# Kernel tuning notes

Hardware: AMD Instinct MI355X
Metric: run time of the kernel (lower is better)

## Reference

```python
import jax, jax.numpy as jnp
import numpy as np

B, S, D, H = 2, 2048, 1024, 16
DK = D // H

def setup_inputs() -> dict:
    key = jax.random.key(0)
    k1, k2, k3 = jax.random.split(key, 3)
    std = 2.0 / (D + 3 * D)
    x = jax.random.normal(k1, (B, S, D), dtype=jnp.float32)
    W_qkv = jax.random.normal(k2, (3 * D, D), dtype=jnp.float32) * std
    W_out = jax.random.normal(k3, (D, D), dtype=jnp.float32) * (2.0 / (2 * D))
    return {"x": x, "W_qkv": W_qkv, "W_out": W_out}

def reference(x, W_qkv, W_out):
    # fused QKV projection: [..., d_in] x [d_out, d_in] -> [..., d_out]
    proj = jnp.einsum('bsd,ed->bse', x, W_qkv)               # [B,S,3*H*DK]
    proj = proj.reshape(B, S, 3, H, DK)
    q = proj[:, :, 0].transpose(0, 2, 1, 3)                  # [B,H,S,DK]
    k = proj[:, :, 1].transpose(0, 2, 1, 3)
    v = proj[:, :, 2].transpose(0, 2, 1, 3)
    scores = jnp.einsum('bhnd,bhmd->bhnm', q, k) / jnp.sqrt(jnp.float32(DK))
    causal = jnp.tril(jnp.ones((S, S), dtype=bool))
    scores = jnp.where(causal, scores, -jnp.inf)
    attn = jax.nn.softmax(scores, axis=-1)
    out = jnp.einsum('bhnm,bhmd->bhnd', attn, v)             # [B,H,S,DK]
    out = out.transpose(0, 2, 1, 3).reshape(B, S, H * DK)
    return jnp.einsum('bsd,ed->bse', out, W_out)             # [B,S,D]
```

## Files before the change

### kernel.cpp

```cpp
#include <hip/hip_runtime.h>
#include <hip/hip_bf16.h>
#include <stdint.h>

typedef __attribute__((ext_vector_type(8)))  __bf16 bf16x8;
typedef __attribute__((ext_vector_type(8)))  short  short8;
typedef __attribute__((ext_vector_type(4)))  float  f32x4;
typedef __attribute__((ext_vector_type(16))) float  f32x16;

#define MFMA16(a, b, c) __builtin_amdgcn_mfma_f32_16x16x32_bf16((a), (b), (c), 0, 0, 0)
#define MFMA32(a, b, c) __builtin_amdgcn_mfma_f32_32x32x16_bf16((a), (b), (c), 0, 0, 0)

__device__ __forceinline__ unsigned short f32_bf16(float f) {
  union { float f; unsigned u; } v; v.f = f;
  unsigned r = v.u + 0x7FFFu + ((v.u >> 16) & 1u);
  return (unsigned short)(r >> 16);
}

__device__ __forceinline__ float fast_exp2(float x) {
#if __has_builtin(__builtin_amdgcn_exp2f)
  return __builtin_amdgcn_exp2f(x);
#else
  return __expf(x * 0.69314718f);
#endif
}

__device__ __forceinline__ void gload16(const unsigned short* g, unsigned short* l) {
  __builtin_amdgcn_global_load_lds(
      (const __attribute__((address_space(1))) unsigned int*)(g),
      (__attribute__((address_space(3))) unsigned int*)(l), 16, 0, 0);
}

__global__ void cvt3_kernel(const float* __restrict__ a, int na4,
                            const float* __restrict__ b, int nb4,
                            const float* __restrict__ c, int nc4,
                            unsigned short* __restrict__ oa,
                            unsigned short* __restrict__ ob,
                            unsigned short* __restrict__ oc) {
  int total = na4 + nb4 + nc4;
  for (int i = blockIdx.x * blockDim.x + threadIdx.x; i < total; i += gridDim.x * blockDim.x) {
    const float* src; unsigned short* dst; int j = i;
    if (j < na4) { src = a; dst = oa; }
    else if (j - na4 < nb4) { j -= na4; src = b; dst = ob; }
    else { j -= na4 + nb4; src = c; dst = oc; }
    float4 v = reinterpret_cast<const float4*>(src)[j];
    ushort4 o4;
    o4.x = f32_bf16(v.x); o4.y = f32_bf16(v.y);
    o4.z = f32_bf16(v.z); o4.w = f32_bf16(v.w);
    reinterpret_cast<ushort4*>(dst)[j] = o4;
  }
}

__global__ __launch_bounds__(512, 2) void gemm_qkv_8ph(const unsigned short* __restrict__ A,
                                                       const unsigned short* __restrict__ Bm,
                                                       unsigned short* __restrict__ qkv) {
  extern __shared__ unsigned short SM[];
  const int tid  = threadIdx.x;
  const int lane = tid & 63;
  const int w    = tid >> 6;
  const int wr   = w >> 2, wc = w & 3;
  const int l16  = lane & 15, lh = lane >> 4;
  const int sw   = l16 & 7;
  const int m0   = blockIdx.y * 256;
  const int n0   = blockIdx.x * 256;

  f32x4 acc[8][4];
#pragma unroll
  for (int mi = 0; mi < 8; ++mi)
#pragma unroll
    for (int ni = 0; ni < 4; ++ni) acc[mi][ni] = 0.f;

  const int r0 = tid >> 3,         h0 = (tid & 7) ^ (r0 & 7);
  const int r1 = (tid + 512) >> 3, h1 = (tid & 7) ^ (r1 & 7);
  const unsigned short* Asrc[2][2];
  const unsigned short* Bsrc[2][2];
  Asrc[0][0] = A + (size_t)(m0 + r0) * 1024 + h0 * 8;
  Asrc[0][1] = A + (size_t)(m0 + r1) * 1024 + h1 * 8;
  Asrc[1][0] = A + (size_t)(m0 + 128 + r0) * 1024 + h0 * 8;
  Asrc[1][1] = A + (size_t)(m0 + 128 + r1) * 1024 + h1 * 8;
  Bsrc[0][0] = Bm + (size_t)(n0 + r0) * 1024 + h0 * 8;
  Bsrc[0][1] = Bm + (size_t)(n0 + r1) * 1024 + h1 * 8;
  Bsrc[1][0] = Bm + (size_t)(n0 + 128 + r0) * 1024 + h0 * 8;
  Bsrc[1][1] = Bm + (size_t)(n0 + 128 + r1) * 1024 + h1 * 8;
  const int ld0 = (w * 64) * 8;
  const int ld1 = (512 + w * 64) * 8;

#define STAGE_A(buf, h, U) do { \
    gload16(Asrc[h][0] + (U) * 64, SM + (buf) * 32768 + (h) * 8192 + ld0); \
    gload16(Asrc[h][1] + (U) * 64, SM + (buf) * 32768 + (h) * 8192 + ld1); } while (0)
#define STAGE_B(buf, h, U) do { \
    gload16(Bsrc[h][0] + (U) * 64, SM + (buf) * 32768 + 16384 + (h) * 8192 + ld0); \
    gload16(Bsrc[h][1] + (U) * 64, SM + (buf) * 32768 + 16384 + (h) * 8192 + ld1); } while (0)

  STAGE_A(0, 0, 0); STAGE_A(0, 1, 0);
  STAGE_B(0, 0, 0); STAGE_B(0, 1, 0);
  STAGE_B(1, 0, 1); STAGE_B(1, 1, 1);
  asm volatile("s_waitcnt vmcnt(4)" ::: "memory");
  __builtin_amdgcn_s_barrier();

  const int NT = 16;
#pragma unroll 2
  for (int U = 0; U < NT; ++U) {
    const int b = U & 1;
    const unsigned short* Ab = SM + b * 32768 + wr * 8192;
    const unsigned short* Bb = SM + b * 32768 + 16384 + (wc >> 1) * 8192;
    const int rB = (wc & 1) * 64;
    bf16x8 bfr[4][2], af[2][2];

#define LDA(i, j) (*(const bf16x8*)(Ab + (((i) * 16 + l16) * 8 + (((j) * 4 + lh) ^ sw)) * 8))
#define LDB(n, j) (*(const bf16x8*)(Bb + (((rB + (n) * 16 + l16)) * 8 + (((j) * 4 + lh) ^ sw)) * 8))
#define PHASE_MFMA(p) \
    __builtin_amdgcn_s_setprio(1); \
    _Pragma("unroll") \
    for (int n = 0; n < 4; ++n) { \
      acc[2*(p)][n]   = MFMA16(af[0][0], bfr[n][0], acc[2*(p)][n]); \
      acc[2*(p)][n]   = MFMA16(af[0][1], bfr[n][1], acc[2*(p)][n]); \
      acc[2*(p)+1][n] = MFMA16(af[1][0], bfr[n][0], acc[2*(p)+1][n]); \
      acc[2*(p)+1][n] = MFMA16(af[1][1], bfr[n][1], acc[2*(p)+1][n]); \
    } \
    __builtin_amdgcn_s_setprio(0);

    af[0][0] = LDA(0, 0); af[0][1] = LDA(0, 1);
    af[1][0] = LDA(1, 0); af[1][1] = LDA(1, 1);
#pragma unroll
    for (int n = 0; n < 4; ++n) { bfr[n][0] = LDB(n, 0); bfr[n][1] = LDB(n, 1); }
    if (U + 1 < NT) STAGE_A(b ^ 1, 0, U + 1);
    __builtin_amdgcn_s_barrier();
    PHASE_MFMA(0)
    __builtin_amdgcn_s_barrier();
    af[0][0] = LDA(2, 0); af[0][1] = LDA(2, 1);
    af[1][0] = LDA(3, 0); af[1][1] = LDA(3, 1);
    if (U + 1 < NT) STAGE_A(b ^ 1, 1, U + 1);
    __builtin_amdgcn_s_barrier();
    PHASE_MFMA(1)
    __builtin_amdgcn_s_barrier();
    af[0][0] = LDA(4, 0); af[0][1] = LDA(4, 1);
    af[1][0] = LDA(5, 0); af[1][1] = LDA(5, 1);
    if (U + 2 < NT) STAGE_B(b, 0, U + 2);
    __builtin_amdgcn_s_barrier();
    PHASE_MFMA(2)
    __builtin_amdgcn_s_barrier();
    af[0][0] = LDA(6, 0); af[0][1] = LDA(6, 1);
    af[1][0] = LDA(7, 0); af[1][1] = LDA(7, 1);
    if (U + 2 < NT) STAGE_B(b, 1, U + 2);
    __builtin_amdgcn_s_barrier();
    PHASE_MFMA(3)
    asm volatile("s_waitcnt vmcnt(4)" ::: "memory");
    __builtin_amdgcn_s_barrier();
#undef LDA
#undef LDB
#undef PHASE_MFMA
  }

  __syncthreads();
  unsigned short* Ep = SM + w * 8192;
  const int gn0 = n0 + wc * 64;
  const int cc  = gn0 >> 10;
  const int hh2 = (gn0 & 1023) >> 6;
  const int gm0 = m0 + wr * 128;
  const int bb2 = gm0 >> 11;
  const int ss0 = gm0 & 2047;
  const int bh2 = bb2 * 16 + hh2;

  if (cc < 2) {
    const float qsc = (cc == 0) ? 0.18033688f : 1.0f;
#pragma unroll
    for (int mi = 0; mi < 8; ++mi)
#pragma unroll
      for (int ni = 0; ni < 4; ++ni)
#pragma unroll
        for (int r = 0; r < 4; ++r) {
          int row = mi * 16 + lh * 4 + r;
          int col = (ni * 16 + l16) ^ (lh << 3);
          Ep[row * 64 + col] = f32_bf16(acc[mi][ni][r] * qsc);
        }
    unsigned short* qk = qkv + (((size_t)cc * 32 + bh2) * 2048 + ss0) * 64;
#pragma unroll
    for (int it = 0; it < 16; ++it) {
      int ci = it * 64 + lane;
      int row = ci >> 3, c = ci & 7;
      short8 vv = *(const short8*)(Ep + row * 64 + ((c ^ ((row >> 2) & 3)) * 8));
      *(short8*)(qk + (size_t)row * 64 + c * 8) = vv;
    }
  } else {
#pragma unroll
    for (int mi = 0; mi < 8; ++mi)
#pragma unroll
      for (int ni = 0; ni < 4; ++ni) {
        int dk = ni * 16 + l16;
        int ssl = mi * 16 + lh * 4;
        unsigned lo, hi;
        asm("v_cvt_pk_bf16_f32 %0, %1, %2" : "=v"(lo) : "v"(acc[mi][ni][0]), "v"(acc[mi][ni][1]));
        asm("v_cvt_pk_bf16_f32 %0, %1, %2" : "=v"(hi) : "v"(acc[mi][ni][2]), "v"(acc[mi][ni][3]));
        int off = dk * 128 + (ssl ^ ((dk & 7) << 3));
        *(uint2*)(Ep + off) = make_uint2(lo, hi);
      }
    unsigned short* vt = qkv + (size_t)8388608 + (size_t)bh2 * 64 * 2048 + ss0;
#pragma unroll
    for (int it = 0; it < 16; ++it) {
      int ci = it * 64 + lane;
      int dk = ci >> 4, c = ci & 15;
      short8 vv = *(const short8*)(Ep + dk * 128 + ((c ^ (dk & 7)) * 8));
      *(short8*)(vt + (size_t)dk * 2048 + c * 8) = vv;
    }
  }
#undef STAGE_A
#undef STAGE_B
}

__global__ __launch_bounds__(256) void gemm_out(const unsigned short* __restrict__ A,
                                                const unsigned short* __restrict__ Bm,
                                                float* __restrict__ C,
                                                int M, int N, int K) {
  extern __shared__ unsigned short SM[];
  unsigned short* As = SM;
  unsigned short* Bs = SM + 2048;
  const int tid  = threadIdx.x;
  const int lane = tid & 63;
  const int wid  = tid >> 6;
  const int l16  = lane & 15, lh = lane >> 4;
  const int m0   = blockIdx.y * 64;
  const int n0   = blockIdx.x * 128;

  f32x4 acc[4][2];
#pragma unroll
  for (int mi = 0; mi < 4; ++mi)
#pragma unroll
    for (int ni = 0; ni < 2; ++ni) acc[mi][ni] = 0.f;

  const unsigned short* aSrc = A + (size_t)(m0 + (tid >> 2)) * K + (tid & 3) * 8;
  const unsigned short* b0   = Bm + (size_t)(n0 + (tid >> 2)) * K + (tid & 3) * 8;
  const unsigned short* b1   = Bm + (size_t)(n0 + 64 + (tid >> 2)) * K + (tid & 3) * 8;
  const int dA  = wid * 512;
  const int dB0 = wid * 512;
  const int dB1 = 2048 + wid * 512;

  for (int k0 = 0; k0 < K; k0 += 32) {
    __syncthreads();
    gload16(aSrc + k0, As + dA);
    gload16(b0 + k0, Bs + dB0);
    gload16(b1 + k0, Bs + dB1);
    __syncthreads();
    bf16x8 af[4], bfr[2];
#pragma unroll
    for (int mi = 0; mi < 4; ++mi)
      af[mi] = *(const bf16x8*)(As + (mi * 16 + l16) * 32 + lh * 8);
#pragma unroll
    for (int ni = 0; ni < 2; ++ni)
      bfr[ni] = *(const bf16x8*)(Bs + (wid * 32 + ni * 16 + l16) * 32 + lh * 8);
#pragma unroll
    for (int mi = 0; mi < 4; ++mi)
#pragma unroll
      for (int ni = 0; ni < 2; ++ni)
        acc[mi][ni] = MFMA16(af[mi], bfr[ni], acc[mi][ni]);
  }

  __syncthreads();
  float* Ef = (float*)SM + wid * 2048;
#pragma unroll
  for (int mi = 0; mi < 4; ++mi)
#pragma unroll
    for (int ni = 0; ni < 2; ++ni)
#pragma unroll
      for (int r = 0; r < 4; ++r) {
        int row = mi * 16 + lh * 4 + r;
        int col = (ni * 16 + l16) ^ ((row & 7) << 2);
        Ef[row * 32 + col] = acc[mi][ni][r];
      }
#pragma unroll
  for (int it = 0; it < 8; ++it) {
    int ci = it * 64 + lane;
    int row = ci >> 3, c4 = ci & 7;
    float4 vv = *(const float4*)(Ef + row * 32 + ((c4 * 4) ^ ((row & 7) << 2)));
    *(float4*)(&C[(size_t)(m0 + row) * N + n0 + wid * 32 + c4 * 4]) = vv;
  }
}

__device__ const signed char JQT[48] = {31,31,30,15, 30,29,29,28,14, 28,27,27,26,13, 26,25,25,24,12,
                                        24,23,23,22,11, 22,21,21,20,10, 20,19,19,18, 9, 18,17,17,16, 8,
                                        16, 7, 6, 5, 4, 3, 2, 1, 0};
__device__ const signed char JS0[48] = { 0,16, 0, 0, 16, 0,15, 0, 0, 15, 0,14, 0, 0, 14, 0,13, 0, 0,
                                        13, 0,12, 0, 0, 12, 0,11, 0, 0, 11, 0,10, 0, 0, 10, 0, 9, 0, 0,
                                         9, 0, 0, 0, 0, 0, 0, 0, 0};
__device__ const signed char JNT[48] = {16,16,16,16, 15,15,15,15,15, 14,14,14,14,14, 13,13,13,13,13,
                                        12,12,12,12,12, 11,11,11,11,11, 10,10,10,10,10,  9, 9, 9, 9, 9,
                                         8, 8, 7, 6, 5, 4, 3, 2, 1};
__device__ const signed char JSL[48] = {30,31,28,-1, 29,26,27,24,-1, 25,22,23,20,-1, 21,18,19,16,-1,
                                        17,14,15,12,-1, 13,10,11, 8,-1,  9, 6, 7, 4,-1,  5, 2, 3, 0,-1,
                                         1,-1,-1,-1,-1,-1,-1,-1,-1};

__global__ __launch_bounds__(256) void attn_kernel(const unsigned short* __restrict__ Qg,
                                                   const unsigned short* __restrict__ Kg,
                                                   const unsigned short* __restrict__ Vtg,
                                                   unsigned short* __restrict__ Og,
                                                   char* __restrict__ parts) {
  __shared__ unsigned short Ks[2][64 * 64];
  __shared__ unsigned short Vs[2][64 * 64];

  const int tid  = threadIdx.x;
  const int lane = tid & 63;
  const int w    = tid >> 6;
  const int wq   = w & 1, wkv = w >> 1;
  const int l31  = lane & 31, hi = lane >> 5;
  const int rx0  = (l31 ^ (l31 >> 3)) & 7;

  const int jb   = blockIdx.x >> 5;
  const int bh   = blockIdx.x & 31;
  const int qt   = JQT[jb];
  const int ts0  = JS0[jb];
  const int tend = ts0 + JNT[jb];
  const int slot = JSL[jb];
  const int bb   = bh >> 4, hh = bh & 15;
  const int qb   = qt * 64;
  const int qcol = qb + wq * 32 + l31;

  const unsigned short* Qh = Qg + (size_t)bh * (2048 * 64);
  const unsigned short* Kh = Kg + (size_t)bh * (2048 * 64);
  const unsigned short* Vh = Vtg + (size_t)bh * (64 * 2048);

  bf16x8 qf[4];
#pragma unroll
  for (int ks = 0; ks < 4; ++ks)
    qf[ks] = *(const bf16x8*)(Qh + (size_t)qcol * 64 + ks * 16 + hi * 8);

  f32x16 o0 = 0.f, o1 = 0.f;
  float mreg = 0.f, ll = 0.f;

  const int sA = tid, sB = tid + 256;
  const int rA = sA >> 3, hA = (sA & 7) ^ ((rA ^ (rA >> 3)) & 7);
  const int rB = sB >> 3, hB = (sB & 7) ^ ((rB ^ (rB >> 3)) & 7);
  const unsigned short* kSrcA = Kh + rA * 64 + hA * 8;
  const unsigned short* kSrcB = Kh + rB * 64 + hB * 8;
  const unsigned short* vSrcA = Vh + (size_t)rA * 2048 + hA * 8;
  const unsigned short* vSrcB = Vh + (size_t)rB * 2048 + hB * 8;
  const int ldsA = (w * 64) * 8;
  const int ldsB = (256 + w * 64) * 8;

  gload16(kSrcA + (size_t)(ts0 * 64) * 64, &Ks[0][ldsA]);
  gload16(kSrcB + (size_t)(ts0 * 64) * 64, &Ks[0][ldsB]);
  gload16(vSrcA + ts0 * 64, &Vs[0][ldsA]);
  gload16(vSrcB + ts0 * 64, &Vs[0][ldsB]);
  __syncthreads();

  const unsigned short* kA = kSrcA + (size_t)(ts0 + 1) * 4096;
  const unsigned short* kB = kSrcB + (size_t)(ts0 + 1) * 4096;
  const unsigned short* vA = vSrcA + (ts0 + 1) * 64;
  const unsigned short* vB = vSrcB + (ts0 + 1) * 64;

  for (int t = ts0; t < tend; ++t) {
    const int kv0 = t * 64;
    const int cur = (t - ts0) & 1;
    if (t + 1 < tend) {
      gload16(kA, &Ks[cur ^ 1][ldsA]);
      gload16(kB, &Ks[cur ^ 1][ldsB]);
      gload16(vA, &Vs[cur ^ 1][ldsA]);
      gload16(vB, &Vs[cur ^ 1][ldsB]);
      kA += 4096; kB += 4096; vA += 64; vB += 64;
    }
    const unsigned short* Kb = Ks[cur];
    const unsigned short* Vb = Vs[cur];

    f32x16 s = 0.f;
    const int kvl = wkv * 32 + l31;
#pragma unroll
    for (int ks = 0; ks < 4; ++ks) {
      int c = (ks * 2 + hi) ^ rx0 ^ (wkv << 2);
      bf16x8 ka = *(const bf16x8*)(Kb + kvl * 64 + c * 8);
      s = MFMA32(ka, qf[ks], s);
    }

    if (t == qt) {
#pragma unroll
      for (int r = 0; r < 16; ++r) {
        int kvp = kv0 + wkv * 32 + (r & 3) + 8 * (r >> 2) + 4 * hi;
        if (kvp > qcol) s[r] = -__builtin_inff();
      }
    }

    float pm = fmaxf(fmaxf(s[0], s[1]), s[2]);
    pm = fmaxf(fmaxf(pm, s[3]), s[4]);
    pm = fmaxf(fmaxf(pm, s[5]), s[6]);
    pm = fmaxf(fmaxf(pm, s[7]), s[8]);
    pm = fmaxf(fmaxf(pm, s[9]), s[10]);
    pm = fmaxf(fmaxf(pm, s[11]), s[12]);
    pm = fmaxf(fmaxf(pm, s[13]), s[14]);
    pm = fmaxf(pm, s[15]);
    if (!__all(pm <= mreg + 8.f)) {
      float t0 = fmaxf(pm, __shfl_xor(pm, 32));
      float mn = fmaxf(mreg, t0);
      float esc = fast_exp2(mreg - mn);
      mreg = mn; ll *= esc;
#pragma unroll
      for (int r = 0; r < 16; ++r) { o0[r] *= esc; o1[r] *= esc; }
    }

    float p[16];
#pragma unroll
    for (int r = 0; r < 16; ++r) p[r] = fast_exp2(s[r] - mreg);
    float ps = ((p[0] + p[1]) + (p[2] + p[3])) + ((p[4] + p[5]) + (p[6] + p[7]))
             + ((p[8] + p[9]) + (p[10] + p[11])) + ((p[12] + p[13]) + (p[14] + p[15]));
    ps += __shfl_xor(ps, 32);
    ll += ps;

    bf16x8 pf[2];
#pragma unroll
    for (int ks = 0; ks < 2; ++ks) {
      const int off = ks * 8;
      unsigned a1, b1, a2, b2;
      asm("v_cvt_pk_bf16_f32 %0, %1, %2" : "=v"(a1) : "v"(p[off + 0]), "v"(p[off + 1]));
      asm("v_cvt_pk_bf16_f32 %0, %1, %2" : "=v"(b1) : "v"(p[off + 4]), "v"(p[off + 5]));
      asm("v_cvt_pk_bf16_f32 %0, %1, %2" : "=v"(a2) : "v"(p[off + 2]), "v"(p[off + 3]));
      asm("v_cvt_pk_bf16_f32 %0, %1, %2" : "=v"(b2) : "v"(p[off + 6]), "v"(p[off + 7]));
      asm("v_permlane32_swap_b32 %0, %1" : "+v"(a1), "+v"(b1));
      asm("v_permlane32_swap_b32 %0, %1" : "+v"(a2), "+v"(b2));
      union { unsigned u[4]; bf16x8 f; } fr;
      fr.u[0] = a1; fr.u[1] = a2; fr.u[2] = b1; fr.u[3] = b2;
      pf[ks] = fr.f;
    }

#pragma unroll
    for (int ks = 0; ks < 2; ++ks) {
      int cbase = wkv * 4 + ks * 2 + hi;
      bf16x8 va0 = *(const bf16x8*)(Vb + l31 * 64 + (cbase ^ rx0) * 8);
      bf16x8 va1 = *(const bf16x8*)(Vb + (32 + l31) * 64 + (cbase ^ rx0 ^ 4) * 8);
      o0 = MFMA32(va0, pf[ks], o0);
      o1 = MFMA32(va1, pf[ks], o1);
    }
    __syncthreads();
  }

  float* oxch = (float*)Ks;
  float* lmx  = (float*)Vs;
  if (wkv == 1) {
    float* dst = oxch + wq * 2048;
#pragma unroll
    for (int r = 0; r < 16; ++r) {
      int d0 = (r & 3) + 8 * (r >> 2) + 4 * hi;
      dst[d0 * 32 + l31] = o0[r];
      dst[(32 + d0) * 32 + l31] = o1[r];
    }
    if (hi == 0) { lmx[wq * 64 + l31] = ll; lmx[wq * 64 + 32 + l31] = mreg; }
  }
  __syncthreads();
  if (wkv == 0) {
    float lB = lmx[wq * 64 + l31];
    float mB = lmx[wq * 64 + 32 + l31];
    float mx = fmaxf(mreg, mB);
    float wA = fast_exp2(mreg - mx), wB = fast_exp2(mB - mx);
    float lT = ll * wA + lB * wB;
    float inv = (slot < 0) ? (1.f / lT) : 1.f;
    float sA2 = wA * inv, sB2 = wB * inv;
    const float* src = oxch + wq * 2048;
    unsigned short* slab = (unsigned short*)((char*)Vs + 1024) + wq * 2048;
#pragma unroll
    for (int i = 0; i < 8; ++i) {
      int r = 2 * i;
      int d0 = (r & 3) + 8 * (r >> 2) + 4 * hi;
      float x0 = o0[r] * sA2 + src[d0 * 32 + l31] * sB2;
      float x1 = o0[r + 1] * sA2 + src[(d0 + 1) * 32 + l31] * sB2;
      float y0 = o1[r] * sA2 + src[(32 + d0) * 32 + l31] * sB2;
      float y1 = o1[r + 1] * sA2 + src[(33 + d0) * 32 + l31] * sB2;
      unsigned u0, u1;
      asm("v_cvt_pk_bf16_f32 %0, %1, %2" : "=v"(u0) : "v"(x0), "v"(x1));
      asm("v_cvt_pk_bf16_f32 %0, %1, %2" : "=v"(u1) : "v"(y0), "v"(y1));
      *(unsigned*)(slab + l31 * 64 + (((d0 >> 3) ^ (l31 & 7)) * 8) + (d0 & 7)) = u0;
      int d1 = 32 + d0;
      *(unsigned*)(slab + l31 * 64 + (((d1 >> 3) ^ (l31 & 7)) * 8) + (d1 & 7)) = u1;
    }
    if (slot < 0) {
      unsigned short* op = Og + (size_t)bb * 2048 * 1024 + (size_t)hh * 64;
#pragma unroll
      for (int it = 0; it < 4; ++it) {
        int ci = it * 64 + lane;
        int qr = ci >> 3, c = ci & 7;
        short8 vv = *(const short8*)(slab + qr * 64 + ((c ^ (qr & 7)) * 8));
        *(short8*)(op + (size_t)(qb + wq * 32 + qr) * 1024 + c * 8) = vv;
      }
    } else {
      char* pb = parts + (size_t)(bh * 32 + slot) * 8704;
      float* pl = (float*)pb;
      float* pmv = pl + 64;
      unsigned short* pO = (unsigned short*)(pb + 512);
      if (hi == 0) { pl[wq * 32 + l31] = lT; pmv[wq * 32 + l31] = mx; }
#pragma unroll
      for (int it = 0; it < 4; ++it) {
        int ci = it * 64 + lane;
        int qr = ci >> 3, c = ci & 7;
        short8 vv = *(const short8*)(slab + qr * 64 + ((c ^ (qr & 7)) * 8));
        *(short8*)(pO + (size_t)(wq * 32 + qr) * 64 + c * 8) = vv;
      }
    }
  }
}

__global__ __launch_bounds__(256) void merge_kernel(const char* __restrict__ parts,
                                                    unsigned short* __restrict__ Og) {
  const int task = blockIdx.x;
  const int bh = task & 31, qi = task >> 5;
  const int qt = 16 + qi;
  const int bb = bh >> 4, hh = bh & 15;
  const int tid = threadIdx.x;
  const int r = tid >> 2, q = tid & 3;

  const char* pb1 = parts + (size_t)(bh * 32 + 2 * qi) * 8704;
  const char* pb2 = parts + (size_t)(bh * 32 + 2 * qi + 1) * 8704;
  const float* l1p = (const float*)pb1;
  const float* l2p = (const float*)pb2;
  float lv1 = l1p[r], mv1 = l1p[64 + r];
  float lv2 = l2p[r], mv2 = l2p[64 + r];
  float mx = fmaxf(mv1, mv2);
  float w1 = fast_exp2(mv1 - mx), w2 = fast_exp2(mv2 - mx);
  float inv = 1.f / (lv1 * w1 + lv2 * w2);
  float s1 = w1 * inv, s2 = w2 * inv;

  const unsigned short* O1 = (const unsigned short*)(pb1 + 512) + r * 64 + q * 16;
  const unsigned short* O2 = (const unsigned short*)(pb2 + 512) + r * 64 + q * 16;
  short8 a0 = *(const short8*)(O1);
  short8 a1 = *(const short8*)(O1 + 8);
  short8 b0 = *(const short8*)(O2);
  short8 b1 = *(const short8*)(O2 + 8);

  unsigned outw[8];
#pragma unroll
  for (int i = 0; i < 4; ++i) {
    float x0 = __builtin_bit_cast(float, ((unsigned)(unsigned short)a0[2 * i]) << 16) * s1 +
               __builtin_bit_cast(float, ((unsigned)(unsigned short)b0[2 * i]) << 16) * s2;
    float x1 = __builtin_bit_cast(float, ((unsigned)(unsigned short)a0[2 * i + 1]) << 16) * s1 +
               __builtin_bit_cast(float, ((unsigned)(unsigned short)b0[2 * i + 1]) << 16) * s2;
    asm("v_cvt_pk_bf16_f32 %0, %1, %2" : "=v"(outw[i]) : "v"(x0), "v"(x1));
    float y0 = __builtin_bit_cast(float, ((unsigned)(unsigned short)a1[2 * i]) << 16) * s1 +
               __builtin_bit_cast(float, ((unsigned)(unsigned short)b1[2 * i]) << 16) * s2;
    float y1 = __builtin_bit_cast(float, ((unsigned)(unsigned short)a1[2 * i + 1]) << 16) * s1 +
               __builtin_bit_cast(float, ((unsigned)(unsigned short)b1[2 * i + 1]) << 16) * s2;
    asm("v_cvt_pk_bf16_f32 %0, %1, %2" : "=v"(outw[4 + i]) : "v"(y0), "v"(y1));
  }
  unsigned short* op = Og + ((size_t)bb * 2048 + qt * 64 + r) * 1024 + hh * 64 + q * 16;
  *(uint4*)(op)     = make_uint4(outw[0], outw[1], outw[2], outw[3]);
  *(uint4*)(op + 8) = make_uint4(outw[4], outw[5], outw[6], outw[7]);
}

extern "C" void kernel_launch(void* const* d_in, const int* in_sizes, int n_in,
                              void* d_out, int out_size, void* d_ws, size_t ws_size,
                              hipStream_t stream) {
  const float* x    = (const float*)d_in[0];
  const float* Wqkv = (const float*)d_in[1];
  const float* Wout = (const float*)d_in[2];
  float* out = (float*)d_out;

  char* ws = (char*)d_ws;
  unsigned short* xb  = (unsigned short*)(ws);
  unsigned short* wqb = (unsigned short*)(ws + (size_t)8 * 1024 * 1024);
  unsigned short* wob = (unsigned short*)(ws + (size_t)14 * 1024 * 1024);
  unsigned short* qkv = (unsigned short*)(ws + (size_t)16 * 1024 * 1024);
  unsigned short* att = (unsigned short*)(ws + (size_t)40 * 1024 * 1024);
  char* parts = ws;

  static bool attr_set = false;
  if (!attr_set) {
    hipFuncSetAttribute((const void*)gemm_qkv_8ph,
                        hipFuncAttributeMaxDynamicSharedMemorySize, 131072);
    attr_set = true;
  }

  cvt3_kernel<<<2048, 256, 0, stream>>>(x, 4194304 / 4, Wqkv, 3145728 / 4,
                                        Wout, 1048576 / 4, xb, wqb, wob);

  gemm_qkv_8ph<<<dim3(12, 16), 512, 131072, stream>>>(xb, wqb, qkv);

  const unsigned short* Qp  = qkv;
  const unsigned short* Kp  = qkv + 4194304;
  const unsigned short* Vtp = qkv + 8388608;
  attn_kernel<<<1536, 256, 0, stream>>>(Qp, Kp, Vtp, att, parts);
  merge_kernel<<<512, 256, 0, stream>>>(parts, att);

  gemm_out<<<dim3(8, 64), 256, 32768, stream>>>(att, wob, out, 4096, 1024, 1024);
}
```

Baseline: 106.8 us.

## Fuse split-KV merge into attention kernel via last-arriver atomic counter

Drops the separate merge kernel launch. Each pair of split-KV attention blocks now increments a per-(head, q-tile) atomic flag, and the second block to arrive combines the two partial outputs and writes the final rows. The flags are zeroed in the conversion kernel. This removes one kernel launch and its tail gap, at the cost of threadfence/atomic overhead and extra work on the tail blocks. It falls back to the old merge kernel if the workspace is too small.

```diff
diff --git a/kernel.cpp b/kernel.cpp
--- a/kernel.cpp
+++ b/kernel.cpp
@@ -35,7 +35,12 @@
                             const float* __restrict__ c, int nc4,
                             unsigned short* __restrict__ oa,
                             unsigned short* __restrict__ ob,
-                            unsigned short* __restrict__ oc) {
+                            unsigned short* __restrict__ oc,
+                            unsigned* __restrict__ flags) {
+  if (flags && blockIdx.x == 0 && threadIdx.x < 256) {
+    flags[threadIdx.x] = 0;
+    flags[threadIdx.x + 256] = 0;
+  }
   int total = na4 + nb4 + nc4;
   for (int i = blockIdx.x * blockDim.x + threadIdx.x; i < total; i += gridDim.x * blockDim.x) {
     const float* src; unsigned short* dst; int j = i;
@@ -292,7 +297,8 @@
                                                    const unsigned short* __restrict__ Kg,
                                                    const unsigned short* __restrict__ Vtg,
                                                    unsigned short* __restrict__ Og,
-                                                   char* __restrict__ parts) {
+                                                   char* __restrict__ parts,
+                                                   unsigned* __restrict__ flags) {
   __shared__ unsigned short Ks[2][64 * 64];
   __shared__ unsigned short Vs[2][64 * 64];
 
@@ -490,6 +496,52 @@
       }
     }
   }
+
+  if (slot >= 0 && flags != nullptr) {
+    const int qi = slot >> 1;
+    __threadfence();
+    __syncthreads();
+    unsigned* bc = (unsigned*)&Ks[0][0];
+    if (tid == 0) *bc = atomicAdd(&flags[bh * 16 + qi], 1u);
+    __syncthreads();
+    if (*bc == 1) {
+      __threadfence();
+      const int r = tid >> 2, q = tid & 3;
+      const char* pb1 = parts + (size_t)(bh * 32 + 2 * qi) * 8704;
+      const char* pb2 = parts + (size_t)(bh * 32 + 2 * qi + 1) * 8704;
+      const float* l1p = (const float*)pb1;
+      const float* l2p = (const float*)pb2;
+      float lv1 = l1p[r], mv1 = l1p[64 + r];
+      float lv2 = l2p[r], mv2 = l2p[64 + r];
+      float mx2 = fmaxf(mv1, mv2);
+      float w1 = fast_exp2(mv1 - mx2), w2 = fast_exp2(mv2 - mx2);
+      float inv2 = 1.f / (lv1 * w1 + lv2 * w2);
+      float s1 = w1 * inv2, s2 = w2 * inv2;
+      const unsigned short* O1 = (const unsigned short*)(pb1 + 512) + r * 64 + q * 16;
+      const unsigned short* O2 = (const unsigned short*)(pb2 + 512) + r * 64 + q * 16;
+      short8 a0 = *(const short8*)(O1);
+      short8 a1v = *(const short8*)(O1 + 8);
+      short8 b0v = *(const short8*)(O2);
+      short8 b1v = *(const short8*)(O2 + 8);
+      unsigned outw[8];
+#pragma unroll
+      for (int i = 0; i < 4; ++i) {
+        float x0 = __builtin_bit_cast(float, ((unsigned)(unsigned short)a0[2 * i]) << 16) * s1 +
+                   __builtin_bit_cast(float, ((unsigned)(unsigned short)b0v[2 * i]) << 16) * s2;
+        float x1 = __builtin_bit_cast(float, ((unsigned)(unsigned short)a0[2 * i + 1]) << 16) * s1 +
+                   __builtin_bit_cast(float, ((unsigned)(unsigned short)b0v[2 * i + 1]) << 16) * s2;
+        asm("v_cvt_pk_bf16_f32 %0, %1, %2" : "=v"(outw[i]) : "v"(x0), "v"(x1));
+        float y0 = __builtin_bit_cast(float, ((unsigned)(unsigned short)a1v[2 * i]) << 16) * s1 +
+                   __builtin_bit_cast(float, ((unsigned)(unsigned short)b1v[2 * i]) << 16) * s2;
+        float y1 = __builtin_bit_cast(float, ((unsigned)(unsigned short)a1v[2 * i + 1]) << 16) * s1 +
+                   __builtin_bit_cast(float, ((unsigned)(unsigned short)b1v[2 * i + 1]) << 16) * s2;
+        asm("v_cvt_pk_bf16_f32 %0, %1, %2" : "=v"(outw[4 + i]) : "v"(y0), "v"(y1));
+      }
+      unsigned short* op = Og + ((size_t)bb * 2048 + (16 + qi) * 64 + r) * 1024 + hh * 64 + q * 16;
+      *(uint4*)(op)     = make_uint4(outw[0], outw[1], outw[2], outw[3]);
+      *(uint4*)(op + 8) = make_uint4(outw[4], outw[5], outw[6], outw[7]);
+    }
+  }
 }
 
 __global__ __launch_bounds__(256) void merge_kernel(const char* __restrict__ parts,
@@ -554,6 +606,10 @@
   unsigned short* att = (unsigned short*)(ws + (size_t)40 * 1024 * 1024);
   char* parts = ws;
 
+  const size_t flagsOff = (size_t)48 * 1024 * 1024;
+  const bool fused = (ws_size >= flagsOff + 4096);
+  unsigned* flags = fused ? (unsigned*)(ws + flagsOff) : nullptr;
+
   static bool attr_set = false;
   if (!attr_set) {
     hipFuncSetAttribute((const void*)gemm_qkv_8ph,
@@ -562,15 +618,15 @@
   }
 
   cvt3_kernel<<<2048, 256, 0, stream>>>(x, 4194304 / 4, Wqkv, 3145728 / 4,
-                                        Wout, 1048576 / 4, xb, wqb, wob);
+                                        Wout, 1048576 / 4, xb, wqb, wob, flags);
 
   gemm_qkv_8ph<<<dim3(12, 16), 512, 131072, stream>>>(xb, wqb, qkv);
 
   const unsigned short* Qp  = qkv;
   const unsigned short* Kp  = qkv + 4194304;
   const unsigned short* Vtp = qkv + 8388608;
-  attn_kernel<<<1536, 256, 0, stream>>>(Qp, Kp, Vtp, att, parts);
-  merge_kernel<<<512, 256, 0, stream>>>(parts, att);
+  attn_kernel<<<1536, 256, 0, stream>>>(Qp, Kp, Vtp, att, parts, flags);
+  if (!fused) merge_kernel<<<512, 256, 0, stream>>>(parts, att);
 
   gemm_out<<<dim3(8, 64), 256, 32768, stream>>>(att, wob, out, 4096, 1024, 1024);
 }
```

Result: slower. 266.6 us (+149.7%).
